# Kernel tuning notes

Measured on AMD Instinct MI355X. Metric: run time of the kernel, lower is better.

The kernel has to match this reference:

```python
import jax, jax.numpy as jnp
import numpy as np
import math

B, N, DHID, NH, DHEAD, DFF = 2, 1024, 512, 16, 32, 2048
FACTOR = 0.5 / math.sqrt(DHEAD)


def _ln(x, g, b):
    m = jnp.mean(x, -1, keepdims=True)
    v = jnp.mean((x - m) ** 2, -1, keepdims=True)
    return (x - m) / jnp.sqrt(v + 1e-5) * g + b


def setup_inputs() -> dict:
    key = jax.random.key(0)
    ks = jax.random.split(key, 16)
    rn = lambda k, s, sc=0.02: jax.random.normal(k, s, jnp.float32) * sc
    inp = {}
    inp["H"] = jax.random.normal(ks[0], (B, N, DHID), jnp.float32)
    inp["V"] = jax.random.normal(ks[1], (B, N, 3, DHID), jnp.float32)
    inp["D"] = jax.random.normal(ks[2], (B, N, N), jnp.float32)
    inp["rbf"] = jax.random.normal(ks[3], (B, NH, N, N), jnp.float32)
    inp["mask"] = jnp.ones((B, N), jnp.int32)
    # attention params
    inp["Wq"] = rn(ks[4], (DHID, 4 * DHID)); inp["bq"] = jnp.zeros(4 * DHID)
    inp["Wk"] = rn(ks[5], (DHID, 4 * DHID)); inp["bk"] = jnp.zeros(4 * DHID)
    inp["Wvs"] = rn(ks[6], (DHID, DHID)); inp["bvs"] = jnp.zeros(DHID)
    inp["Wvv"] = rn(ks[7], (DHID, DHID))
    inp["Wo"] = rn(ks[8], (DHID, DHID)); inp["bo"] = jnp.zeros(DHID)
    inp["Wvo"] = rn(ks[9], (DHID, DHID))
    inp["ln1_g"] = jnp.ones(DHID); inp["ln1_b"] = jnp.zeros(DHID)
    # GVP FFN params
    inp["Wlv"] = rn(ks[10], (DHID, 2 * DHID))
    inp["W1"] = rn(ks[11], (2 * DHID, DFF)); inp["b1"] = jnp.zeros(DFF)
    inp["W2"] = rn(ks[12], (DFF, 2 * DHID)); inp["b2"] = jnp.zeros(2 * DHID)
    inp["ln2_g"] = jnp.ones(DHID); inp["ln2_b"] = jnp.zeros(DHID)
    return inp


def reference(H, V, D, rbf, mask, Wq, bq, Wk, bk, Wvs, bvs, Wvv, Wo, bo, Wvo,
              ln1_g, ln1_b, Wlv, W1, b1, W2, b2, ln2_g, ln2_b):
    # ---- self-attention sublayer (pre-LN on H only, residual on H and V) ----
    Hn = _ln(H, ln1_g, ln1_b)
    Hq = (Hn @ Wq + bq).reshape(B, N, NH, 4 * DHEAD)
    Hk = (Hn @ Wk + bk).reshape(B, N, NH, 4 * DHEAD)
    Hv = (Hn @ Wvs + bvs).reshape(B, N, NH, DHEAD)
    # vector values: (B,N,3,DHID) -> (B,N,3,NH,DHEAD) -> (B,N,NH,3,DHEAD) -> (B,N,NH,3*DHEAD)
    Vv = (V @ Wvv).reshape(B, N, 3, NH, DHEAD).transpose(0, 1, 3, 2, 4).reshape(B, N, NH, 3 * DHEAD)
    V_attn = jnp.concatenate([Hv, Vv], axis=-1)  # (B,N,NH,4*DHEAD)
    bias = rbf + D[:, None]  # (B,NH,N,N)
    bias = jnp.where((mask[:, None, None, :] == 0), -jnp.inf, bias)
    scores = jnp.einsum('bnhd,bmhd->bhnm', Hq, Hk) * FACTOR + bias
    attn = jax.nn.softmax(scores, axis=-1)
    res = jnp.einsum('bhnm,bmhd->bnhd', attn, V_attn)  # (B,N,NH,4*DHEAD)
    H_res = res[..., :DHEAD].reshape(B, N, DHID)
    V_res = res[..., DHEAD:].reshape(B, N, NH, 3, DHEAD).transpose(0, 1, 3, 2, 4).reshape(B, N, 3, DHID)
    H = H + (H_res @ Wo + bo)
    V = V + (V_res @ Wvo)
    # ---- GVP FFN sublayer (pre-LN on H only, residual) ----
    Hn = _ln(H, ln2_g, ln2_b)
    Vp = V @ Wlv  # (B,N,3, 2*DHID)
    V1, V2 = Vp[..., :DHID], Vp[..., DHID:]
    scaler = jnp.concatenate([Hn, jnp.linalg.norm(V1, axis=-2)], axis=-1)  # (B,N,2*DHID)
    s = jax.nn.silu(scaler @ W1 + b1) @ W2 + b2  # (B,N,2*DHID)
    H_out, V_upd = s[..., :DHID], s[..., DHID:]
    H = H + H_out
    V = V + V_upd[:, :, None, :] * V2  # vector_act='none'
    return (H, V)
```

## Files before the change

kernel.cpp:

```cpp
#include <hip/hip_runtime.h>
#include <math.h>

constexpr int Bc = 2, Nseq = 1024, Dh = 512, Nh = 16, Dhead = 32;
constexpr float FACT = 0.08838834764831845f;
constexpr float LOG2E = 1.4426950408889634f;

typedef __attribute__((ext_vector_type(8))) __bf16 bf16x8;
typedef __attribute__((ext_vector_type(4))) float f32x4;

__device__ __forceinline__ short f2b(float x) {
    union { float f; unsigned u; } v; v.f = x;
    unsigned r = v.u + 0x7fffu + ((v.u >> 16) & 1u);
    return (short)(r >> 16);
}
__device__ __forceinline__ float b2f(short s) {
    union { unsigned u; float f; } v; v.u = ((unsigned)(unsigned short)s) << 16;
    return v.f;
}

#define GL2LDS(g, s) __builtin_amdgcn_global_load_lds(                  \
    (const void __attribute__((address_space(1)))*)(g),                 \
    (void __attribute__((address_space(3)))*)(s), 16, 0, 0)

__device__ __forceinline__ void mfma_loop(const short* __restrict__ A, int lda,
                                          const short* __restrict__ B, int ldb,
                                          int K, short* __restrict__ smA,
                                          short* __restrict__ smB, f32x4 acc[4][4]) {
    const int tid = threadIdx.x;
    const int lane = tid & 63;
    const int w = tid >> 6;
    const int wr = (w >> 1) * 64, wc = (w & 1) * 64;
    const int lr = lane & 15;
    const int srow = tid >> 3;
    const int scol = tid & 7;
    for (int k0 = 0; k0 < K; k0 += 64) {
        __syncthreads();
#pragma unroll
        for (int r = 0; r < 4; r++) {
            int row = r * 32 + srow;
            int gc = scol ^ (row & 7);
            GL2LDS(A + (long)row * lda + k0 + gc * 8, smA + row * 64 + scol * 8);
            GL2LDS(B + (long)row * ldb + k0 + gc * 8, smB + row * 64 + scol * 8);
        }
        __syncthreads();
#pragma unroll
        for (int h = 0; h < 2; h++) {
            int cb = h * 4 + (lane >> 4);
            bf16x8 af[4], bv[4];
#pragma unroll
            for (int i = 0; i < 4; i++) {
                int row = wr + i * 16 + lr;
                af[i] = *(const bf16x8*)(smA + row * 64 + ((cb ^ (row & 7)) << 3));
            }
#pragma unroll
            for (int j = 0; j < 4; j++) {
                int row = wc + j * 16 + lr;
                bv[j] = *(const bf16x8*)(smB + row * 64 + ((cb ^ (row & 7)) << 3));
            }
            __builtin_amdgcn_s_setprio(1);
#pragma unroll
            for (int i = 0; i < 4; i++)
#pragma unroll
                for (int j = 0; j < 4; j++)
                    acc[i][j] = __builtin_amdgcn_mfma_f32_16x16x32_bf16(af[i], bv[j], acc[i][j], 0, 0, 0);
            __builtin_amdgcn_s_setprio(0);
        }
    }
}

__global__ __launch_bounds__(256) void gemm_bf16(
    const short* __restrict__ A, int lda, long sAz,
    const short* __restrict__ B, int ldb, long sBz,
    void* __restrict__ C, int ldc, long sCz,
    const float* __restrict__ bias,
    const float* __restrict__ resid, int ldr, long sRz,
    short* __restrict__ aux,
    int K, int flags)
{
    __shared__ short smA[128 * 64], smB[128 * 64];
    const long z = blockIdx.z;
    const short* Ab = A + z * sAz + (long)blockIdx.y * 128 * lda;
    const short* Bb = B + z * sBz + (long)blockIdx.x * 128 * ldb;
    f32x4 acc[4][4] = {};
    mfma_loop(Ab, lda, Bb, ldb, K, smA, smB, acc);
    const int tid = threadIdx.x, lane = tid & 63, w = tid >> 6;
    const int wr = (w >> 1) * 64, wc = (w & 1) * 64, lr = lane & 15, r0 = (lane >> 4) * 4;
    const int m0 = blockIdx.y * 128, n0 = blockIdx.x * 128;
    float* Cf = (float*)C; short* Cs = (short*)C;
    const float* rz = resid ? resid + z * sRz : nullptr;
#pragma unroll
    for (int i = 0; i < 4; i++)
#pragma unroll
        for (int j = 0; j < 4; j++) {
            int col = n0 + wc + j * 16 + lr;
            float bv = bias ? bias[col] : 0.f;
#pragma unroll
            for (int q = 0; q < 4; q++) {
                int row = m0 + wr + i * 16 + r0 + q;
                float c = acc[i][j][q] + bv;
                if (rz) c += rz[(long)row * ldr + col];
                if (flags & 1) c = c / (1.f + __expf(-c));
                long off = z * sCz + (long)row * ldc + col;
                if (flags & 2) Cs[off] = f2b(c); else Cf[off] = c;
                if (aux) aux[off] = f2b(c);
            }
        }
}

__global__ __launch_bounds__(256) void gemm_qkv_vvv(
    const short* __restrict__ Hn, const short* __restrict__ WqkvT,
    const short* __restrict__ Vbf, const short* __restrict__ WvvT,
    short* __restrict__ Hqkv, short* __restrict__ VvR,
    const float* __restrict__ bqkv)
{
    __shared__ short smA[128 * 64], smB[128 * 64];
    const bool qkv = blockIdx.y < 16;
    if (!qkv && blockIdx.x >= 4) return;
    const int yy = qkv ? blockIdx.y : blockIdx.y - 16;
    const short* Ab = (qkv ? Hn : Vbf) + (long)yy * 128 * 512;
    const short* Bb = (qkv ? WqkvT : WvvT) + (long)blockIdx.x * 128 * 512;
    f32x4 acc[4][4] = {};
    mfma_loop(Ab, 512, Bb, 512, 512, smA, smB, acc);
    const int tid = threadIdx.x, lane = tid & 63, w = tid >> 6;
    const int wr = (w >> 1) * 64, wc = (w & 1) * 64, lr = lane & 15, r0 = (lane >> 4) * 4;
    const int m0 = yy * 128, n0 = blockIdx.x * 128;
    short* Cs = qkv ? Hqkv : VvR;
    const int ldc = qkv ? 4608 : 512;
#pragma unroll
    for (int i = 0; i < 4; i++)
#pragma unroll
        for (int j = 0; j < 4; j++) {
            int col = n0 + wc + j * 16 + lr;
            float bv = qkv ? bqkv[col] : 0.f;
#pragma unroll
            for (int q = 0; q < 4; q++) {
                int row = m0 + wr + i * 16 + r0 + q;
                Cs[(long)row * ldc + col] = f2b(acc[i][j][q] + bv);
            }
        }
}

__global__ __launch_bounds__(256) void gemm_out(
    const short* __restrict__ Ares, const short* __restrict__ WoT,
    const short* __restrict__ WvoT, float* __restrict__ outHV,
    const float* __restrict__ H, const float* __restrict__ V,
    short* __restrict__ Vbf2, const float* __restrict__ bo)
{
    __shared__ short smA[128 * 64], smB[128 * 64];
    const bool isH = blockIdx.y < 16;
    const short* Ab = Ares + (long)blockIdx.y * 128 * 512;
    const short* Bb = (isH ? WoT : WvoT) + (long)blockIdx.x * 128 * 512;
    f32x4 acc[4][4] = {};
    mfma_loop(Ab, 512, Bb, 512, 512, smA, smB, acc);
    const int tid = threadIdx.x, lane = tid & 63, w = tid >> 6;
    const int wr = (w >> 1) * 64, wc = (w & 1) * 64, lr = lane & 15, r0 = (lane >> 4) * 4;
    const int m0 = blockIdx.y * 128, n0 = blockIdx.x * 128;
#pragma unroll
    for (int i = 0; i < 4; i++)
#pragma unroll
        for (int j = 0; j < 4; j++) {
            int col = n0 + wc + j * 16 + lr;
            float bv = isH ? bo[col] : 0.f;
#pragma unroll
            for (int q = 0; q < 4; q++) {
                int row = m0 + wr + i * 16 + r0 + q;
                float c = acc[i][j][q] + bv;
                if (isH) c += H[(long)row * 512 + col];
                else     c += V[(long)(row - 2048) * 512 + col];
                outHV[(long)row * 512 + col] = c;
                if (!isH) Vbf2[(long)(row - 2048) * 512 + col] = f2b(c);
            }
        }
}

__global__ __launch_bounds__(256, 2) void flash_attn(
    const short* __restrict__ Hq, const short* __restrict__ Hk,
    const short* __restrict__ VaT, const float* __restrict__ rbf,
    const float* __restrict__ Dm, const float* __restrict__ maskadd,
    short* __restrict__ Hres, short* __restrict__ Vres, int ldq)
{
    __shared__ short smK[128 * 128];
    __shared__ short smV[128 * 128];
    __shared__ short smP[4 * 16 * 128];
    const int xcd = blockIdx.x & 7, idx = blockIdx.x >> 3;
    const int s = (idx >> 4) * 8 + xcd;
    const int qt = idx & 15;
    const int b = s >> 4, h = s & 15;
    const int q0 = qt * 64;
    const int tid = threadIdx.x, lane = tid & 63, w = tid >> 6;
    const int lr = lane & 15, hi = lane >> 4, r0 = hi * 4;
    const int c16 = tid & 15, rS = tid >> 4;
    short* smPw = smP + w * 2048;

    bf16x8 qf[4];
    {
        const short* qb = Hq + ((long)b * Nseq + q0 + w * 16 + lr) * ldq + h * 128 + hi * 8;
#pragma unroll
        for (int kk = 0; kk < 4; kk++) qf[kk] = *(const bf16x8*)(qb + kk * 32);
    }

    f32x4 oac[8] = {};
    float ml[4], ll[4];
#pragma unroll
    for (int q = 0; q < 4; q++) { ml[q] = -INFINITY; ll[q] = 0.f; }

    const short* Kg = Hk + (long)b * Nseq * ldq + h * 128;
    const short* Vg = VaT + (long)s * 128 * Nseq;
    const float* rbb = rbf + ((long)s * Nseq + q0 + w * 16) * Nseq;
    const float* Dbb = Dm + ((long)b * Nseq + q0 + w * 16) * Nseq;
    const float* mab = maskadd + b * Nseq;
    const int bcol = (lane & 31) * 4, brow2 = lane >> 5;

    for (int kt = 0; kt < 8; kt++) {
        __syncthreads();
        {
            bf16x8 t8[8];
#pragma unroll
            for (int r = 0; r < 8; r++)
                t8[r] = *(const bf16x8*)(Kg + (long)(kt * 128 + rS + r * 16) * ldq + c16 * 8);
#pragma unroll
            for (int r = 0; r < 8; r++) {
                int row = rS + r * 16;
                *(bf16x8*)(smK + row * 128 + (c16 ^ (row & 15)) * 8) = t8[r];
            }
#pragma unroll
            for (int r = 0; r < 8; r++)
                t8[r] = *(const bf16x8*)(Vg + (long)(rS + r * 16) * Nseq + kt * 128 + c16 * 8);
#pragma unroll
            for (int r = 0; r < 8; r++) {
                int row = rS + r * 16;
                *(bf16x8*)(smV + row * 128 + (c16 ^ (row & 15)) * 8) = t8[r];
            }
        }
        {
            short4 hb[8];
            float4 mk = *(const float4*)(mab + kt * 128 + bcol);
#pragma unroll
            for (int it = 0; it < 8; it++) {
                int row = it * 2 + brow2;
                float4 rv = *(const float4*)(rbb + (long)row * Nseq + kt * 128 + bcol);
                float4 dv = *(const float4*)(Dbb + (long)row * Nseq + kt * 128 + bcol);
                hb[it].x = f2b((rv.x + dv.x + mk.x) * LOG2E);
                hb[it].y = f2b((rv.y + dv.y + mk.y) * LOG2E);
                hb[it].z = f2b((rv.z + dv.z + mk.z) * LOG2E);
                hb[it].w = f2b((rv.w + dv.w + mk.w) * LOG2E);
            }
            int ch = bcol >> 3;
#pragma unroll
            for (int it = 0; it < 8; it++) {
                int row = it * 2 + brow2;
                *(short4*)(smPw + row * 128 + ((ch ^ (row & 7)) << 3) + (bcol & 7)) = hb[it];
            }
        }
        __syncthreads();

        f32x4 sac[8] = {};
#pragma unroll
        for (int kk = 0; kk < 4; kk++) {
            int cb = kk * 4 + hi;
            bf16x8 kv8[8];
#pragma unroll
            for (int j = 0; j < 8; j++) {
                int row = j * 16 + lr;
                kv8[j] = *(const bf16x8*)(smK + row * 128 + ((cb ^ (row & 15)) << 3));
            }
#pragma unroll
            for (int j = 0; j < 8; j++)
                sac[j] = __builtin_amdgcn_mfma_f32_16x16x32_bf16(qf[kk], kv8[j], sac[j], 0, 0, 0);
        }
        float tmax[4];
#pragma unroll
        for (int q = 0; q < 4; q++) tmax[q] = -INFINITY;
#pragma unroll
        for (int j = 0; j < 8; j++) {
            int col = j * 16 + lr;
            int ch = col >> 3, in8 = col & 7;
#pragma unroll
            for (int q = 0; q < 4; q++) {
                int row = r0 + q;
                float x = sac[j][q] + b2f(smPw[row * 128 + ((ch ^ (row & 7)) << 3) + in8]);
                sac[j][q] = x;
                tmax[q] = fmaxf(tmax[q], x);
            }
        }
#pragma unroll
        for (int st = 1; st < 16; st <<= 1)
#pragma unroll
            for (int q = 0; q < 4; q++) tmax[q] = fmaxf(tmax[q], __shfl_xor(tmax[q], st));
        float dm = -INFINITY;
#pragma unroll
        for (int q = 0; q < 4; q++) dm = fmaxf(dm, tmax[q] - ml[q]);
        if (!__all(dm <= 8.f)) {
#pragma unroll
            for (int q = 0; q < 4; q++) {
                float mn = fmaxf(ml[q], tmax[q]);
                float sc = exp2f(ml[q] - mn);
                ml[q] = mn;
                ll[q] *= sc;
#pragma unroll
                for (int j = 0; j < 8; j++) oac[j][q] *= sc;
            }
        }
        float rsum[4] = {0.f, 0.f, 0.f, 0.f};
#pragma unroll
        for (int j = 0; j < 8; j++)
#pragma unroll
            for (int q = 0; q < 4; q++) {
                float p = exp2f(sac[j][q] - ml[q]);
                sac[j][q] = p;
                rsum[q] += p;
            }
#pragma unroll
        for (int st = 1; st < 16; st <<= 1)
#pragma unroll
            for (int q = 0; q < 4; q++) rsum[q] += __shfl_xor(rsum[q], st);
#pragma unroll
        for (int q = 0; q < 4; q++) ll[q] += rsum[q];
#pragma unroll
        for (int j = 0; j < 8; j++) {
            int col = j * 16 + lr;
            int ch = col >> 3, in8 = col & 7;
#pragma unroll
            for (int q = 0; q < 4; q++) {
                int row = r0 + q;
                smPw[row * 128 + ((ch ^ (row & 7)) << 3) + in8] = f2b(sac[j][q]);
            }
        }
#pragma unroll
        for (int kk = 0; kk < 4; kk++) {
            int cb = kk * 4 + hi;
            bf16x8 paf = *(const bf16x8*)(smPw + lr * 128 + ((cb ^ (lr & 7)) << 3));
            bf16x8 vv[8];
#pragma unroll
            for (int j = 0; j < 8; j++) {
                int row = j * 16 + lr;
                vv[j] = *(const bf16x8*)(smV + row * 128 + ((cb ^ (row & 15)) << 3));
            }
#pragma unroll
            for (int j = 0; j < 8; j++)
                oac[j] = __builtin_amdgcn_mfma_f32_16x16x32_bf16(paf, vv[j], oac[j], 0, 0, 0);
        }
    }
    float inv[4];
#pragma unroll
    for (int q = 0; q < 4; q++) inv[q] = 1.f / ll[q];
#pragma unroll
    for (int j = 0; j < 8; j++) {
        int d = j * 16 + lr;
#pragma unroll
        for (int q = 0; q < 4; q++) {
            int n = q0 + w * 16 + r0 + q;
            float o = oac[j][q] * inv[q];
            if (d < 32) Hres[((long)b * Nseq + n) * 512 + h * 32 + d] = f2b(o);
            else {
                int c3 = (d - 32) >> 5, dd = (d - 32) & 31;
                Vres[(((long)b * Nseq + n) * 3 + c3) * 512 + h * 32 + dd] = f2b(o);
            }
        }
    }
}

struct PrepJobs {
    const float* W[9];
    short* Wt[9];
    int K[9], N[9], nx[9], base[9];
    float scale[9];
    int base_convk, base_bprep, base_mask;
    const float* V; short* Vbf;
    const float* bq; const float* bk; const float* bvs; float* bqkv;
    const int* mask; float* maskadd;
};

__global__ __launch_bounds__(256) void prep_k(PrepJobs a) {
    int bid = blockIdx.x;
    int tid = threadIdx.x;
    if (bid >= a.base_convk) {
        if (bid < a.base_bprep) {
            int i = (bid - a.base_convk) * 256 + tid;
            float4 v = ((const float4*)a.V)[i];
            short4 s;
            s.x = f2b(v.x); s.y = f2b(v.y); s.z = f2b(v.z); s.w = f2b(v.w);
            ((short4*)a.Vbf)[i] = s;
        } else if (bid < a.base_mask) {
            int i = (bid - a.base_bprep) * 256 + tid;
            float v;
            if (i < 2048) v = a.bq[i] * (FACT * LOG2E);
            else if (i < 4096) v = a.bk[i - 2048];
            else v = a.bvs[i - 4096];
            a.bqkv[i] = v;
        } else {
            int i = (bid - a.base_mask) * 256 + tid;
            a.maskadd[i] = a.mask[i] ? 0.f : -1e30f;
        }
        return;
    }
    int j = 0;
#pragma unroll
    for (int t = 1; t < 9; t++) j = (bid >= a.base[t]) ? t : j;
    const float* W = a.W[j];
    short* Wt = a.Wt[j];
    int K = a.K[j], N = a.N[j];
    float scale = a.scale[j];
    int local = bid - a.base[j];
    int nx = a.nx[j];
    int bx = local % nx, by = local / nx;
    __shared__ float t[32][33];
    int n0 = bx * 32, k0 = by * 32;
    int tx = tid & 31, ty = tid >> 5;
#pragma unroll
    for (int r = 0; r < 4; r++) t[ty + r * 8][tx] = W[(long)(k0 + ty + r * 8) * N + n0 + tx];
    __syncthreads();
#pragma unroll
    for (int r = 0; r < 4; r++) Wt[(long)(n0 + ty + r * 8) * K + k0 + tx] = f2b(t[tx][ty + r * 8] * scale);
}

__device__ __forceinline__ void stv(float* p, float v) { *p = v; }
__device__ __forceinline__ void stv(short* p, float v) { *p = f2b(v); }

template <typename OT>
__global__ __launch_bounds__(256) void ln_kernel(const float* __restrict__ x,
                                                 const float* __restrict__ g,
                                                 const float* __restrict__ b,
                                                 OT* __restrict__ y, int ldo) {
    int row = blockIdx.x;
    const float* xr = x + (long)row * Dh;
    OT* yr = y + (long)row * ldo;
    int tid = threadIdx.x;
    float v0 = xr[tid], v1 = xr[tid + 256];
    __shared__ float red[256];
    red[tid] = v0 + v1;
    __syncthreads();
    for (int o = 128; o > 0; o >>= 1) { if (tid < o) red[tid] += red[tid + o]; __syncthreads(); }
    float mean = red[0] * (1.0f / Dh);
    __syncthreads();
    float d0 = v0 - mean, d1 = v1 - mean;
    red[tid] = d0 * d0 + d1 * d1;
    __syncthreads();
    for (int o = 128; o > 0; o >>= 1) { if (tid < o) red[tid] += red[tid + o]; __syncthreads(); }
    float rstd = rsqrtf(red[0] * (1.0f / Dh) + 1e-5f);
    stv(&yr[tid], d0 * rstd * g[tid] + b[tid]);
    stv(&yr[tid + 256], d1 * rstd * g[tid + 256] + b[tid + 256]);
}

__global__ __launch_bounds__(256) void vattn_t8(const short* __restrict__ Hv, int ldh,
                                                const short* __restrict__ Vv,
                                                short* __restrict__ VaT) {
    int idx = blockIdx.x * 256 + threadIdx.x;
    int m = idx & 1023;
    int c = (idx >> 10) & 15;
    int s = idx >> 14;
    int b = s >> 4, h = s & 15;
    bf16x8 v;
    if (c < 4) {
        v = *(const bf16x8*)(Hv + ((long)b * Nseq + m) * ldh + h * 32 + c * 8);
    } else {
        int c3 = (c - 4) >> 2, dd = ((c - 4) & 3) * 8;
        v = *(const bf16x8*)(Vv + (((long)b * Nseq + m) * 3 + c3) * 512 + h * 32 + dd);
    }
    short* out = VaT + (long)s * 128 * 1024 + (long)c * 8 * 1024 + m;
    const short* vs = (const short*)&v;
#pragma unroll
    for (int e = 0; e < 8; e++) out[e * 1024] = vs[e];
}

__global__ __launch_bounds__(256) void scaler_norm(const float* __restrict__ Vp,
                                                   short* __restrict__ scaler) {
    int idx = blockIdx.x * 256 + threadIdx.x;
    int jj = (idx & 127) * 4;
    int row = idx >> 7;
    float4 ss = {0.f, 0.f, 0.f, 0.f};
#pragma unroll
    for (int c = 0; c < 3; c++) {
        float4 v = *(const float4*)(Vp + ((long)row * 3 + c) * 1024 + jj);
        ss.x += v.x * v.x; ss.y += v.y * v.y; ss.z += v.z * v.z; ss.w += v.w * v.w;
    }
    short4 o;
    o.x = f2b(sqrtf(ss.x)); o.y = f2b(sqrtf(ss.y));
    o.z = f2b(sqrtf(ss.z)); o.w = f2b(sqrtf(ss.w));
    *(short4*)(scaler + (long)row * 1024 + 512 + jj) = o;
}

__global__ __launch_bounds__(256) void final_k(float* __restrict__ outH,
                                               float* __restrict__ outV,
                                               const float* __restrict__ s,
                                               const float* __restrict__ Vp) {
    int idx = blockIdx.x * 256 + threadIdx.x;
    int jj = (idx & 127) * 4;
    int row = idx >> 7;
    float4 s1 = *(const float4*)(s + (long)row * 1024 + jj);
    float4 h = *(const float4*)(outH + (long)row * 512 + jj);
    h.x += s1.x; h.y += s1.y; h.z += s1.z; h.w += s1.w;
    *(float4*)(outH + (long)row * 512 + jj) = h;
    float4 vu = *(const float4*)(s + (long)row * 1024 + 512 + jj);
#pragma unroll
    for (int c = 0; c < 3; c++) {
        float4 v2 = *(const float4*)(Vp + ((long)row * 3 + c) * 1024 + 512 + jj);
        float* vp = outV + ((long)row * 3 + c) * 512 + jj;
        float4 vo = *(const float4*)vp;
        vo.x += vu.x * v2.x; vo.y += vu.y * v2.y;
        vo.z += vu.z * v2.z; vo.w += vu.w * v2.w;
        *(float4*)vp = vo;
    }
}

extern "C" void kernel_launch(void* const* d_in, const int* in_sizes, int n_in,
                              void* d_out, int out_size, void* d_ws, size_t ws_size,
                              hipStream_t stream) {
    const float* H    = (const float*)d_in[0];
    const float* V    = (const float*)d_in[1];
    const float* Dm   = (const float*)d_in[2];
    const float* rbf  = (const float*)d_in[3];
    const int*   mask = (const int*)d_in[4];
    const float* Wq   = (const float*)d_in[5];
    const float* bq   = (const float*)d_in[6];
    const float* Wk   = (const float*)d_in[7];
    const float* bk   = (const float*)d_in[8];
    const float* Wvs  = (const float*)d_in[9];
    const float* bvs  = (const float*)d_in[10];
    const float* Wvv  = (const float*)d_in[11];
    const float* Wo   = (const float*)d_in[12];
    const float* bo   = (const float*)d_in[13];
    const float* Wvo  = (const float*)d_in[14];
    const float* ln1g = (const float*)d_in[15];
    const float* ln1b = (const float*)d_in[16];
    const float* Wlv  = (const float*)d_in[17];
    const float* W1   = (const float*)d_in[18];
    const float* b1   = (const float*)d_in[19];
    const float* W2   = (const float*)d_in[20];
    const float* b2   = (const float*)d_in[21];
    const float* ln2g = (const float*)d_in[22];
    const float* ln2b = (const float*)d_in[23];

    char* wsb = (char*)d_ws;
    auto KB = [&](long kb) { return (void*)(wsb + kb * 1024l); };
    short* WqkvT = (short*)KB(0);
    short* WvvT  = (short*)KB(4608);
    short* WoT   = (short*)KB(5120);
    short* WvoT  = (short*)KB(5632);
    short* WlvT  = (short*)KB(6144);
    short* W1T   = (short*)KB(7168);
    short* W2T   = (short*)KB(11264);
    float* bqkv  = (float*)KB(15360);
    short* Hqkv = (short*)KB(15384);
    short* VvR  = (short*)KB(33816);
    short* VaT  = (short*)KB(39960);
    short* Hn   = (short*)KB(48152);
    short* Vbf  = (short*)KB(50200);
    short* Hres = (short*)KB(56344);
    short* Vres = (short*)KB(58392);
    float* maskadd = (float*)KB(64536);
    short* Vbf2   = (short*)KB(15384);
    float* Vp     = (float*)KB(21528);
    short* scaler = (short*)KB(46104);
    short* t1     = (short*)KB(50200);
    float* sbuf   = (float*)KB(58392);

    float* outH = (float*)d_out;
    float* outV = outH + (size_t)Bc * Nseq * Dh;

    PrepJobs a;
    const float* srcs[9] = {Wq, Wk, Wvs, Wvv, Wo, Wvo, Wlv, W1, W2};
    short* dsts[9] = {WqkvT, WqkvT + 2048 * 512, WqkvT + 4096 * 512,
                      WvvT, WoT, WvoT, WlvT, W1T, W2T};
    int Ks[9] = {512, 512, 512, 512, 512, 512, 512, 1024, 2048};
    int Ns[9] = {2048, 2048, 512, 512, 512, 512, 1024, 2048, 1024};
    float scl[9] = {FACT * LOG2E, 1.f, 1.f, 1.f, 1.f, 1.f, 1.f, 1.f, 1.f};
    int base = 0;
    for (int j = 0; j < 9; j++) {
        a.W[j] = srcs[j]; a.Wt[j] = dsts[j];
        a.K[j] = Ks[j]; a.N[j] = Ns[j];
        a.nx[j] = Ns[j] / 32;
        a.scale[j] = scl[j];
        a.base[j] = base;
        base += (Ns[j] / 32) * (Ks[j] / 32);
    }
    a.base_convk = base;
    a.base_bprep = base + 3072;
    a.base_mask  = base + 3072 + 18;
    a.V = V; a.Vbf = Vbf;
    a.bq = bq; a.bk = bk; a.bvs = bvs; a.bqkv = bqkv;
    a.mask = mask; a.maskadd = maskadd;
    int prep_blocks = a.base_mask + 8;
    prep_k<<<prep_blocks, 256, 0, stream>>>(a);

    ln_kernel<short><<<2048, 256, 0, stream>>>(H, ln1g, ln1b, Hn, 512);
    gemm_qkv_vvv<<<dim3(36, 64), 256, 0, stream>>>(Hn, WqkvT, Vbf, WvvT, Hqkv, VvR, bqkv);
    vattn_t8<<<2048, 256, 0, stream>>>(Hqkv + 4096, 4608, VvR, VaT);

    flash_attn<<<dim3(512), 256, 0, stream>>>(Hqkv, Hqkv + 2048, VaT, rbf, Dm, maskadd,
                                              Hres, Vres, 4608);

    gemm_out<<<dim3(4, 64), 256, 0, stream>>>(Hres, WoT, WvoT, outH, H, V, Vbf2, bo);
    ln_kernel<short><<<2048, 256, 0, stream>>>(outH, ln2g, ln2b, scaler, 1024);
    gemm_bf16<<<dim3(8, 48, 1), 256, 0, stream>>>(Vbf2, 512, 0, WlvT, 512, 0, Vp, 1024, 0,
                                                  nullptr, nullptr, 0, 0, nullptr, 512, 0);
    scaler_norm<<<1024, 256, 0, stream>>>(Vp, scaler);
    gemm_bf16<<<dim3(16, 16, 1), 256, 0, stream>>>(scaler, 1024, 0, W1T, 1024, 0, t1, 2048, 0,
                                                   b1, nullptr, 0, 0, nullptr, 1024, 3);
    gemm_bf16<<<dim3(8, 16, 1), 256, 0, stream>>>(t1, 2048, 0, W2T, 2048, 0, sbuf, 1024, 0,
                                                  b2, nullptr, 0, 0, nullptr, 2048, 0);
    final_k<<<1024, 256, 0, stream>>>(outH, outV, sbuf, Vp);
}
```

Baseline: 255.6 us.

## Shrink flash-attention key tile to 64, fuse W2 GEMM with final residual, bf16 Vp

The flash attention kernel now steps through keys in tiles of 64 instead of 128, which halves the shared-memory footprint and per-iteration register arrays, likely to raise occupancy. The W2 GEMM epilogue now applies the H residual and the V gating update in place, removing the separate final kernel and the fp32 intermediate buffer. The Vp projection is stored in bf16 instead of fp32, cutting traffic for the norm and gating reads at some precision cost. The fused epilogue does scattered read-modify-write accesses, and the attention loop now runs twice as many iterations, each with its own barriers.

New measurement: 278.8 us. +9.1%, slower.

```diff
diff --git a/kernel.cpp b/kernel.cpp
--- a/kernel.cpp
+++ b/kernel.cpp
@@ -173,15 +173,53 @@
         }
 }
 
+__global__ __launch_bounds__(256) void gemm_w2f(
+    const short* __restrict__ t1, const short* __restrict__ W2T,
+    const float* __restrict__ b2, float* __restrict__ outH,
+    float* __restrict__ outV, const short* __restrict__ VpB)
+{
+    __shared__ short smA[128 * 64], smB[128 * 64];
+    const short* Ab = t1 + (long)blockIdx.y * 128 * 2048;
+    const short* Bb = W2T + (long)blockIdx.x * 128 * 2048;
+    f32x4 acc[4][4] = {};
+    mfma_loop(Ab, 2048, Bb, 2048, 2048, smA, smB, acc);
+    const int tid = threadIdx.x, lane = tid & 63, w = tid >> 6;
+    const int wr = (w >> 1) * 64, wc = (w & 1) * 64, lr = lane & 15, r0 = (lane >> 4) * 4;
+    const int m0 = blockIdx.y * 128, n0 = blockIdx.x * 128;
+#pragma unroll
+    for (int i = 0; i < 4; i++)
+#pragma unroll
+        for (int j = 0; j < 4; j++) {
+            int col = n0 + wc + j * 16 + lr;
+            float bv = b2[col];
+#pragma unroll
+            for (int q = 0; q < 4; q++) {
+                int row = m0 + wr + i * 16 + r0 + q;
+                float val = acc[i][j][q] + bv;
+                if (col < 512) {
+                    outH[(long)row * 512 + col] += val;
+                } else {
+                    int cc = col - 512;
+#pragma unroll
+                    for (int c = 0; c < 3; c++) {
+                        long r3 = (long)row * 3 + c;
+                        float v2 = b2f(VpB[r3 * 1024 + 512 + cc]);
+                        outV[r3 * 512 + cc] += val * v2;
+                    }
+                }
+            }
+        }
+}
+
 __global__ __launch_bounds__(256, 2) void flash_attn(
     const short* __restrict__ Hq, const short* __restrict__ Hk,
     const short* __restrict__ VaT, const float* __restrict__ rbf,
     const float* __restrict__ Dm, const float* __restrict__ maskadd,
     short* __restrict__ Hres, short* __restrict__ Vres, int ldq)
 {
-    __shared__ short smK[128 * 128];
-    __shared__ short smV[128 * 128];
-    __shared__ short smP[4 * 16 * 128];
+    __shared__ short smK[64 * 128];
+    __shared__ short smV[128 * 64];
+    __shared__ short smP[4 * 16 * 64];
     const int xcd = blockIdx.x & 7, idx = blockIdx.x >> 3;
     const int s = (idx >> 4) * 8 + xcd;
     const int qt = idx & 15;
@@ -190,7 +228,8 @@
     const int tid = threadIdx.x, lane = tid & 63, w = tid >> 6;
     const int lr = lane & 15, hi = lane >> 4, r0 = hi * 4;
     const int c16 = tid & 15, rS = tid >> 4;
-    short* smPw = smP + w * 2048;
+    const int c8 = tid & 7, rS8 = tid >> 3;
+    short* smPw = smP + w * 1024;
 
     bf16x8 qf[4];
     {
@@ -209,37 +248,37 @@
     const float* rbb = rbf + ((long)s * Nseq + q0 + w * 16) * Nseq;
     const float* Dbb = Dm + ((long)b * Nseq + q0 + w * 16) * Nseq;
     const float* mab = maskadd + b * Nseq;
-    const int bcol = (lane & 31) * 4, brow2 = lane >> 5;
-
-    for (int kt = 0; kt < 8; kt++) {
+    const int bcol = (lane & 15) * 4, brow = lane >> 4;
+
+    for (int kt = 0; kt < 16; kt++) {
         __syncthreads();
         {
-            bf16x8 t8[8];
-#pragma unroll
-            for (int r = 0; r < 8; r++)
-                t8[r] = *(const bf16x8*)(Kg + (long)(kt * 128 + rS + r * 16) * ldq + c16 * 8);
-#pragma unroll
-            for (int r = 0; r < 8; r++) {
+            bf16x8 t8[4];
+#pragma unroll
+            for (int r = 0; r < 4; r++)
+                t8[r] = *(const bf16x8*)(Kg + (long)(kt * 64 + rS + r * 16) * ldq + c16 * 8);
+#pragma unroll
+            for (int r = 0; r < 4; r++) {
                 int row = rS + r * 16;
-                *(bf16x8*)(smK + row * 128 + (c16 ^ (row & 15)) * 8) = t8[r];
-            }
-#pragma unroll
-            for (int r = 0; r < 8; r++)
-                t8[r] = *(const bf16x8*)(Vg + (long)(rS + r * 16) * Nseq + kt * 128 + c16 * 8);
-#pragma unroll
-            for (int r = 0; r < 8; r++) {
-                int row = rS + r * 16;
-                *(bf16x8*)(smV + row * 128 + (c16 ^ (row & 15)) * 8) = t8[r];
+                *(bf16x8*)(smK + row * 128 + ((c16 ^ (row & 15)) << 3)) = t8[r];
+            }
+#pragma unroll
+            for (int r = 0; r < 4; r++)
+                t8[r] = *(const bf16x8*)(Vg + (long)(rS8 + r * 32) * Nseq + kt * 64 + c8 * 8);
+#pragma unroll
+            for (int r = 0; r < 4; r++) {
+                int row = rS8 + r * 32;
+                *(bf16x8*)(smV + row * 64 + ((c8 ^ (row & 7)) << 3)) = t8[r];
             }
         }
         {
-            short4 hb[8];
-            float4 mk = *(const float4*)(mab + kt * 128 + bcol);
-#pragma unroll
-            for (int it = 0; it < 8; it++) {
-                int row = it * 2 + brow2;
-                float4 rv = *(const float4*)(rbb + (long)row * Nseq + kt * 128 + bcol);
-                float4 dv = *(const float4*)(Dbb + (long)row * Nseq + kt * 128 + bcol);
+            short4 hb[4];
+            float4 mk = *(const float4*)(mab + kt * 64 + bcol);
+#pragma unroll
+            for (int it = 0; it < 4; it++) {
+                int row = it * 4 + brow;
+                float4 rv = *(const float4*)(rbb + (long)row * Nseq + kt * 64 + bcol);
+                float4 dv = *(const float4*)(Dbb + (long)row * Nseq + kt * 64 + bcol);
                 hb[it].x = f2b((rv.x + dv.x + mk.x) * LOG2E);
                 hb[it].y = f2b((rv.y + dv.y + mk.y) * LOG2E);
                 hb[it].z = f2b((rv.z + dv.z + mk.z) * LOG2E);
@@ -247,38 +286,38 @@
             }
             int ch = bcol >> 3;
 #pragma unroll
-            for (int it = 0; it < 8; it++) {
-                int row = it * 2 + brow2;
-                *(short4*)(smPw + row * 128 + ((ch ^ (row & 7)) << 3) + (bcol & 7)) = hb[it];
+            for (int it = 0; it < 4; it++) {
+                int row = it * 4 + brow;
+                *(short4*)(smPw + row * 64 + ((ch ^ (row & 7)) << 3) + (bcol & 7)) = hb[it];
             }
         }
         __syncthreads();
 
-        f32x4 sac[8] = {};
+        f32x4 sac[4] = {};
 #pragma unroll
         for (int kk = 0; kk < 4; kk++) {
             int cb = kk * 4 + hi;
-            bf16x8 kv8[8];
-#pragma unroll
-            for (int j = 0; j < 8; j++) {
+            bf16x8 kv8[4];
+#pragma unroll
+            for (int j = 0; j < 4; j++) {
                 int row = j * 16 + lr;
                 kv8[j] = *(const bf16x8*)(smK + row * 128 + ((cb ^ (row & 15)) << 3));
             }
 #pragma unroll
-            for (int j = 0; j < 8; j++)
+            for (int j = 0; j < 4; j++)
                 sac[j] = __builtin_amdgcn_mfma_f32_16x16x32_bf16(qf[kk], kv8[j], sac[j], 0, 0, 0);
         }
         float tmax[4];
 #pragma unroll
         for (int q = 0; q < 4; q++) tmax[q] = -INFINITY;
 #pragma unroll
-        for (int j = 0; j < 8; j++) {
+        for (int j = 0; j < 4; j++) {
             int col = j * 16 + lr;
             int ch = col >> 3, in8 = col & 7;
 #pragma unroll
             for (int q = 0; q < 4; q++) {
                 int row = r0 + q;
-                float x = sac[j][q] + b2f(smPw[row * 128 + ((ch ^ (row & 7)) << 3) + in8]);
+                float x = sac[j][q] + b2f(smPw[row * 64 + ((ch ^ (row & 7)) << 3) + in8]);
                 sac[j][q] = x;
                 tmax[q] = fmaxf(tmax[q], x);
             }
@@ -303,7 +342,7 @@
         }
         float rsum[4] = {0.f, 0.f, 0.f, 0.f};
 #pragma unroll
-        for (int j = 0; j < 8; j++)
+        for (int j = 0; j < 4; j++)
 #pragma unroll
             for (int q = 0; q < 4; q++) {
                 float p = exp2f(sac[j][q] - ml[q]);
@@ -317,24 +356,24 @@
 #pragma unroll
         for (int q = 0; q < 4; q++) ll[q] += rsum[q];
 #pragma unroll
-        for (int j = 0; j < 8; j++) {
+        for (int j = 0; j < 4; j++) {
             int col = j * 16 + lr;
             int ch = col >> 3, in8 = col & 7;
 #pragma unroll
             for (int q = 0; q < 4; q++) {
                 int row = r0 + q;
-                smPw[row * 128 + ((ch ^ (row & 7)) << 3) + in8] = f2b(sac[j][q]);
-            }
-        }
-#pragma unroll
-        for (int kk = 0; kk < 4; kk++) {
+                smPw[row * 64 + ((ch ^ (row & 7)) << 3) + in8] = f2b(sac[j][q]);
+            }
+        }
+#pragma unroll
+        for (int kk = 0; kk < 2; kk++) {
             int cb = kk * 4 + hi;
-            bf16x8 paf = *(const bf16x8*)(smPw + lr * 128 + ((cb ^ (lr & 7)) << 3));
+            bf16x8 paf = *(const bf16x8*)(smPw + lr * 64 + ((cb ^ (lr & 7)) << 3));
             bf16x8 vv[8];
 #pragma unroll
             for (int j = 0; j < 8; j++) {
                 int row = j * 16 + lr;
-                vv[j] = *(const bf16x8*)(smV + row * 128 + ((cb ^ (row & 15)) << 3));
+                vv[j] = *(const bf16x8*)(smV + row * 64 + ((cb ^ (row & 7)) << 3));
             }
 #pragma unroll
             for (int j = 0; j < 8; j++)
@@ -463,44 +502,22 @@
     for (int e = 0; e < 8; e++) out[e * 1024] = vs[e];
 }
 
-__global__ __launch_bounds__(256) void scaler_norm(const float* __restrict__ Vp,
+__global__ __launch_bounds__(256) void scaler_norm(const short* __restrict__ VpB,
                                                    short* __restrict__ scaler) {
     int idx = blockIdx.x * 256 + threadIdx.x;
     int jj = (idx & 127) * 4;
     int row = idx >> 7;
-    float4 ss = {0.f, 0.f, 0.f, 0.f};
+    float ss0 = 0.f, ss1 = 0.f, ss2 = 0.f, ss3 = 0.f;
 #pragma unroll
     for (int c = 0; c < 3; c++) {
-        float4 v = *(const float4*)(Vp + ((long)row * 3 + c) * 1024 + jj);
-        ss.x += v.x * v.x; ss.y += v.y * v.y; ss.z += v.z * v.z; ss.w += v.w * v.w;
+        short4 v = *(const short4*)(VpB + ((long)row * 3 + c) * 1024 + jj);
+        float x0 = b2f(v.x), x1 = b2f(v.y), x2 = b2f(v.z), x3 = b2f(v.w);
+        ss0 += x0 * x0; ss1 += x1 * x1; ss2 += x2 * x2; ss3 += x3 * x3;
     }
     short4 o;
-    o.x = f2b(sqrtf(ss.x)); o.y = f2b(sqrtf(ss.y));
-    o.z = f2b(sqrtf(ss.z)); o.w = f2b(sqrtf(ss.w));
+    o.x = f2b(sqrtf(ss0)); o.y = f2b(sqrtf(ss1));
+    o.z = f2b(sqrtf(ss2)); o.w = f2b(sqrtf(ss3));
     *(short4*)(scaler + (long)row * 1024 + 512 + jj) = o;
-}
-
-__global__ __launch_bounds__(256) void final_k(float* __restrict__ outH,
-                                               float* __restrict__ outV,
-                                               const float* __restrict__ s,
-                                               const float* __restrict__ Vp) {
-    int idx = blockIdx.x * 256 + threadIdx.x;
-    int jj = (idx & 127) * 4;
-    int row = idx >> 7;
-    float4 s1 = *(const float4*)(s + (long)row * 1024 + jj);
-    float4 h = *(const float4*)(outH + (long)row * 512 + jj);
-    h.x += s1.x; h.y += s1.y; h.z += s1.z; h.w += s1.w;
-    *(float4*)(outH + (long)row * 512 + jj) = h;
-    float4 vu = *(const float4*)(s + (long)row * 1024 + 512 + jj);
-#pragma unroll
-    for (int c = 0; c < 3; c++) {
-        float4 v2 = *(const float4*)(Vp + ((long)row * 3 + c) * 1024 + 512 + jj);
-        float* vp = outV + ((long)row * 3 + c) * 512 + jj;
-        float4 vo = *(const float4*)vp;
-        vo.x += vu.x * v2.x; vo.y += vu.y * v2.y;
-        vo.z += vu.z * v2.z; vo.w += vu.w * v2.w;
-        *(float4*)vp = vo;
-    }
 }
 
 extern "C" void kernel_launch(void* const* d_in, const int* in_sizes, int n_in,
@@ -550,10 +567,9 @@
     short* Vres = (short*)KB(58392);
     float* maskadd = (float*)KB(64536);
     short* Vbf2   = (short*)KB(15384);
-    float* Vp     = (float*)KB(21528);
+    short* VpB    = (short*)KB(21528);
     short* scaler = (short*)KB(46104);
     short* t1     = (short*)KB(50200);
-    float* sbuf   = (float*)KB(58392);
 
     float* outH = (float*)d_out;
     float* outV = outH + (size_t)Bc * Nseq * Dh;
@@ -592,12 +608,10 @@
 
     gemm_out<<<dim3(4, 64), 256, 0, stream>>>(Hres, WoT, WvoT, outH, H, V, Vbf2, bo);
     ln_kernel<short><<<2048, 256, 0, stream>>>(outH, ln2g, ln2b, scaler, 1024);
-    gemm_bf16<<<dim3(8, 48, 1), 256, 0, stream>>>(Vbf2, 512, 0, WlvT, 512, 0, Vp, 1024, 0,
-                                                  nullptr, nullptr, 0, 0, nullptr, 512, 0);
-    scaler_norm<<<1024, 256, 0, stream>>>(Vp, scaler);
+    gemm_bf16<<<dim3(8, 48, 1), 256, 0, stream>>>(Vbf2, 512, 0, WlvT, 512, 0, VpB, 1024, 0,
+                                                  nullptr, nullptr, 0, 0, nullptr, 512, 2);
+    scaler_norm<<<1024, 256, 0, stream>>>(VpB, scaler);
     gemm_bf16<<<dim3(16, 16, 1), 256, 0, stream>>>(scaler, 1024, 0, W1T, 1024, 0, t1, 2048, 0,
                                                    b1, nullptr, 0, 0, nullptr, 1024, 3);
-    gemm_bf16<<<dim3(8, 16, 1), 256, 0, stream>>>(t1, 2048, 0, W2T, 2048, 0, sbuf, 1024, 0,
-                                                  b2, nullptr, 0, 0, nullptr, 2048, 0);
-    final_k<<<1024, 256, 0, stream>>>(outH, outV, sbuf, Vp);
-}
+    gemm_w2f<<<dim3(8, 16), 256, 0, stream>>>(t1, W2T, b2, outH, outV, VpB);
+}
```

## Split attention KV range across two blocks and merge partials in separate kernel

Applied to the files above, without the earlier changes.

Flash attention now splits each query tile's 1024 keys into two halves handled by separate blocks (1024 blocks instead of 512), with KV tiles shrunk from 128 to 64 keys. Each block writes unnormalized bf16 partial outputs plus running max and sum, and a new merge kernel combines them and scatters the result into Hres/Vres. The aim is more parallelism and occupancy from the smaller LDS footprint on the large attention stage. The cost is an extra kernel launch, partial-output traffic, and an extra bf16 rounding of the unnormalized partials.

Result: slower. 274.6 us (+7.5%).

```diff
diff --git a/kernel.cpp b/kernel.cpp
--- a/kernel.cpp
+++ b/kernel.cpp
@@ -177,20 +177,24 @@
     const short* __restrict__ Hq, const short* __restrict__ Hk,
     const short* __restrict__ VaT, const float* __restrict__ rbf,
     const float* __restrict__ Dm, const float* __restrict__ maskadd,
-    short* __restrict__ Hres, short* __restrict__ Vres, int ldq)
+    short* __restrict__ Opart, float* __restrict__ mpart,
+    float* __restrict__ lpart, int ldq)
 {
-    __shared__ short smK[128 * 128];
-    __shared__ short smV[128 * 128];
-    __shared__ short smP[4 * 16 * 128];
+    __shared__ short smK[64 * 128];
+    __shared__ short smV[128 * 64];
+    __shared__ short smP[4 * 16 * 64];
     const int xcd = blockIdx.x & 7, idx = blockIdx.x >> 3;
-    const int s = (idx >> 4) * 8 + xcd;
-    const int qt = idx & 15;
+    const int s = (idx >> 5) * 8 + xcd;
+    const int qt = (idx >> 1) & 15;
+    const int p = idx & 1;
     const int b = s >> 4, h = s & 15;
     const int q0 = qt * 64;
+    const int kb0 = p * 512;
     const int tid = threadIdx.x, lane = tid & 63, w = tid >> 6;
     const int lr = lane & 15, hi = lane >> 4, r0 = hi * 4;
     const int c16 = tid & 15, rS = tid >> 4;
-    short* smPw = smP + w * 2048;
+    const int c8 = tid & 7, rS8 = tid >> 3;
+    short* smPw = smP + w * 1024;
 
     bf16x8 qf[4];
     {
@@ -209,37 +213,38 @@
     const float* rbb = rbf + ((long)s * Nseq + q0 + w * 16) * Nseq;
     const float* Dbb = Dm + ((long)b * Nseq + q0 + w * 16) * Nseq;
     const float* mab = maskadd + b * Nseq;
-    const int bcol = (lane & 31) * 4, brow2 = lane >> 5;
+    const int bcol = (lane & 15) * 4, brow = lane >> 4;
 
     for (int kt = 0; kt < 8; kt++) {
+        const int kv0 = kb0 + kt * 64;
         __syncthreads();
         {
-            bf16x8 t8[8];
-#pragma unroll
-            for (int r = 0; r < 8; r++)
-                t8[r] = *(const bf16x8*)(Kg + (long)(kt * 128 + rS + r * 16) * ldq + c16 * 8);
-#pragma unroll
-            for (int r = 0; r < 8; r++) {
+            bf16x8 t8[4];
+#pragma unroll
+            for (int r = 0; r < 4; r++)
+                t8[r] = *(const bf16x8*)(Kg + (long)(kv0 + rS + r * 16) * ldq + c16 * 8);
+#pragma unroll
+            for (int r = 0; r < 4; r++) {
                 int row = rS + r * 16;
-                *(bf16x8*)(smK + row * 128 + (c16 ^ (row & 15)) * 8) = t8[r];
-            }
-#pragma unroll
-            for (int r = 0; r < 8; r++)
-                t8[r] = *(const bf16x8*)(Vg + (long)(rS + r * 16) * Nseq + kt * 128 + c16 * 8);
-#pragma unroll
-            for (int r = 0; r < 8; r++) {
-                int row = rS + r * 16;
-                *(bf16x8*)(smV + row * 128 + (c16 ^ (row & 15)) * 8) = t8[r];
+                *(bf16x8*)(smK + row * 128 + ((c16 ^ (row & 15)) << 3)) = t8[r];
+            }
+#pragma unroll
+            for (int r = 0; r < 4; r++)
+                t8[r] = *(const bf16x8*)(Vg + (long)(rS8 + r * 32) * Nseq + kv0 + c8 * 8);
+#pragma unroll
+            for (int r = 0; r < 4; r++) {
+                int row = rS8 + r * 32;
+                *(bf16x8*)(smV + row * 64 + ((c8 ^ (row & 7)) << 3)) = t8[r];
             }
         }
         {
-            short4 hb[8];
-            float4 mk = *(const float4*)(mab + kt * 128 + bcol);
-#pragma unroll
-            for (int it = 0; it < 8; it++) {
-                int row = it * 2 + brow2;
-                float4 rv = *(const float4*)(rbb + (long)row * Nseq + kt * 128 + bcol);
-                float4 dv = *(const float4*)(Dbb + (long)row * Nseq + kt * 128 + bcol);
+            short4 hb[4];
+            float4 mk = *(const float4*)(mab + kv0 + bcol);
+#pragma unroll
+            for (int it = 0; it < 4; it++) {
+                int row = it * 4 + brow;
+                float4 rv = *(const float4*)(rbb + (long)row * Nseq + kv0 + bcol);
+                float4 dv = *(const float4*)(Dbb + (long)row * Nseq + kv0 + bcol);
                 hb[it].x = f2b((rv.x + dv.x + mk.x) * LOG2E);
                 hb[it].y = f2b((rv.y + dv.y + mk.y) * LOG2E);
                 hb[it].z = f2b((rv.z + dv.z + mk.z) * LOG2E);
@@ -247,38 +252,38 @@
             }
             int ch = bcol >> 3;
 #pragma unroll
-            for (int it = 0; it < 8; it++) {
-                int row = it * 2 + brow2;
-                *(short4*)(smPw + row * 128 + ((ch ^ (row & 7)) << 3) + (bcol & 7)) = hb[it];
+            for (int it = 0; it < 4; it++) {
+                int row = it * 4 + brow;
+                *(short4*)(smPw + row * 64 + ((ch ^ (row & 7)) << 3) + (bcol & 7)) = hb[it];
             }
         }
         __syncthreads();
 
-        f32x4 sac[8] = {};
+        f32x4 sac[4] = {};
 #pragma unroll
         for (int kk = 0; kk < 4; kk++) {
             int cb = kk * 4 + hi;
-            bf16x8 kv8[8];
-#pragma unroll
-            for (int j = 0; j < 8; j++) {
+            bf16x8 kv8[4];
+#pragma unroll
+            for (int j = 0; j < 4; j++) {
                 int row = j * 16 + lr;
                 kv8[j] = *(const bf16x8*)(smK + row * 128 + ((cb ^ (row & 15)) << 3));
             }
 #pragma unroll
-            for (int j = 0; j < 8; j++)
+            for (int j = 0; j < 4; j++)
                 sac[j] = __builtin_amdgcn_mfma_f32_16x16x32_bf16(qf[kk], kv8[j], sac[j], 0, 0, 0);
         }
         float tmax[4];
 #pragma unroll
         for (int q = 0; q < 4; q++) tmax[q] = -INFINITY;
 #pragma unroll
-        for (int j = 0; j < 8; j++) {
+        for (int j = 0; j < 4; j++) {
             int col = j * 16 + lr;
             int ch = col >> 3, in8 = col & 7;
 #pragma unroll
             for (int q = 0; q < 4; q++) {
                 int row = r0 + q;
-                float x = sac[j][q] + b2f(smPw[row * 128 + ((ch ^ (row & 7)) << 3) + in8]);
+                float x = sac[j][q] + b2f(smPw[row * 64 + ((ch ^ (row & 7)) << 3) + in8]);
                 sac[j][q] = x;
                 tmax[q] = fmaxf(tmax[q], x);
             }
@@ -303,12 +308,12 @@
         }
         float rsum[4] = {0.f, 0.f, 0.f, 0.f};
 #pragma unroll
-        for (int j = 0; j < 8; j++)
+        for (int j = 0; j < 4; j++)
 #pragma unroll
             for (int q = 0; q < 4; q++) {
-                float p = exp2f(sac[j][q] - ml[q]);
-                sac[j][q] = p;
-                rsum[q] += p;
+                float pp = exp2f(sac[j][q] - ml[q]);
+                sac[j][q] = pp;
+                rsum[q] += pp;
             }
 #pragma unroll
         for (int st = 1; st < 16; st <<= 1)
@@ -317,46 +322,80 @@
 #pragma unroll
         for (int q = 0; q < 4; q++) ll[q] += rsum[q];
 #pragma unroll
-        for (int j = 0; j < 8; j++) {
+        for (int j = 0; j < 4; j++) {
             int col = j * 16 + lr;
             int ch = col >> 3, in8 = col & 7;
 #pragma unroll
             for (int q = 0; q < 4; q++) {
                 int row = r0 + q;
-                smPw[row * 128 + ((ch ^ (row & 7)) << 3) + in8] = f2b(sac[j][q]);
-            }
-        }
-#pragma unroll
-        for (int kk = 0; kk < 4; kk++) {
+                smPw[row * 64 + ((ch ^ (row & 7)) << 3) + in8] = f2b(sac[j][q]);
+            }
+        }
+#pragma unroll
+        for (int kk = 0; kk < 2; kk++) {
             int cb = kk * 4 + hi;
-            bf16x8 paf = *(const bf16x8*)(smPw + lr * 128 + ((cb ^ (lr & 7)) << 3));
+            bf16x8 paf = *(const bf16x8*)(smPw + lr * 64 + ((cb ^ (lr & 7)) << 3));
             bf16x8 vv[8];
 #pragma unroll
             for (int j = 0; j < 8; j++) {
                 int row = j * 16 + lr;
-                vv[j] = *(const bf16x8*)(smV + row * 128 + ((cb ^ (row & 15)) << 3));
+                vv[j] = *(const bf16x8*)(smV + row * 64 + ((cb ^ (row & 7)) << 3));
             }
 #pragma unroll
             for (int j = 0; j < 8; j++)
                 oac[j] = __builtin_amdgcn_mfma_f32_16x16x32_bf16(paf, vv[j], oac[j], 0, 0, 0);
         }
     }
-    float inv[4];
-#pragma unroll
-    for (int q = 0; q < 4; q++) inv[q] = 1.f / ll[q];
+    const int g = s * 16 + qt;
+    short* Op = Opart + ((long)(p * 512 + g) * 64) * 128;
 #pragma unroll
     for (int j = 0; j < 8; j++) {
         int d = j * 16 + lr;
 #pragma unroll
         for (int q = 0; q < 4; q++) {
-            int n = q0 + w * 16 + r0 + q;
-            float o = oac[j][q] * inv[q];
-            if (d < 32) Hres[((long)b * Nseq + n) * 512 + h * 32 + d] = f2b(o);
-            else {
-                int c3 = (d - 32) >> 5, dd = (d - 32) & 31;
-                Vres[(((long)b * Nseq + n) * 3 + c3) * 512 + h * 32 + dd] = f2b(o);
-            }
-        }
+            int row = w * 16 + r0 + q;
+            Op[(long)row * 128 + d] = f2b(oac[j][q]);
+        }
+    }
+    if (lr == 0) {
+#pragma unroll
+        for (int q = 0; q < 4; q++) {
+            long off = (long)(p * 512 + g) * 64 + w * 16 + r0 + q;
+            mpart[off] = ml[q];
+            lpart[off] = ll[q];
+        }
+    }
+}
+
+__global__ __launch_bounds__(256) void merge_k(
+    const short* __restrict__ Opart, const float* __restrict__ mpart,
+    const float* __restrict__ lpart, short* __restrict__ Hres,
+    short* __restrict__ Vres)
+{
+    int idx = blockIdx.x * 256 + threadIdx.x;
+    int dc = idx & 31, row = (idx >> 5) & 63, g = idx >> 11;
+    int d = dc * 4;
+    long off = (long)g * 64 + row;
+    float m0 = mpart[off], m1 = mpart[512l * 64 + off];
+    float l0 = lpart[off], l1 = lpart[512l * 64 + off];
+    float mm = fmaxf(m0, m1);
+    float w0 = exp2f(m0 - mm), w1 = exp2f(m1 - mm);
+    float inv = 1.f / (l0 * w0 + l1 * w1);
+    short4 a4 = *(const short4*)(Opart + ((long)g * 64 + row) * 128 + d);
+    short4 b4 = *(const short4*)(Opart + ((long)(512 + g) * 64 + row) * 128 + d);
+    short4 o;
+    o.x = f2b((b2f(a4.x) * w0 + b2f(b4.x) * w1) * inv);
+    o.y = f2b((b2f(a4.y) * w0 + b2f(b4.y) * w1) * inv);
+    o.z = f2b((b2f(a4.z) * w0 + b2f(b4.z) * w1) * inv);
+    o.w = f2b((b2f(a4.w) * w0 + b2f(b4.w) * w1) * inv);
+    int s = g >> 4, qt = g & 15;
+    int b = s >> 4, h = s & 15;
+    int n = qt * 64 + row;
+    if (d < 32) {
+        *(short4*)(Hres + ((long)b * Nseq + n) * 512 + h * 32 + d) = o;
+    } else {
+        int c3 = (d - 32) >> 5, dd = (d - 32) & 31;
+        *(short4*)(Vres + (((long)b * Nseq + n) * 3 + c3) * 512 + h * 32 + dd) = o;
     }
 }
 
@@ -549,6 +588,9 @@
     short* Hres = (short*)KB(56344);
     short* Vres = (short*)KB(58392);
     float* maskadd = (float*)KB(64536);
+    short* Opart = (short*)KB(67000);
+    float* mpart = (float*)KB(83500);
+    float* lpart = (float*)KB(83800);
     short* Vbf2   = (short*)KB(15384);
     float* Vp     = (float*)KB(21528);
     short* scaler = (short*)KB(46104);
@@ -587,8 +629,9 @@
     gemm_qkv_vvv<<<dim3(36, 64), 256, 0, stream>>>(Hn, WqkvT, Vbf, WvvT, Hqkv, VvR, bqkv);
     vattn_t8<<<2048, 256, 0, stream>>>(Hqkv + 4096, 4608, VvR, VaT);
 
-    flash_attn<<<dim3(512), 256, 0, stream>>>(Hqkv, Hqkv + 2048, VaT, rbf, Dm, maskadd,
-                                              Hres, Vres, 4608);
+    flash_attn<<<dim3(1024), 256, 0, stream>>>(Hqkv, Hqkv + 2048, VaT, rbf, Dm, maskadd,
+                                               Opart, mpart, lpart, 4608);
+    merge_k<<<4096, 256, 0, stream>>>(Opart, mpart, lpart, Hres, Vres);
 
     gemm_out<<<dim3(4, 64), 256, 0, stream>>>(Hres, WoT, WvoT, outH, H, V, Vbf2, bo);
     ln_kernel<short><<<2048, 256, 0, stream>>>(outH, ln2g, ln2b, scaler, 1024);
```
